# Kernel tuning notes

Hardware: AMD Instinct MI355X
Metric: run time of the kernel (lower is better)

Reference implementation:

```python
import jax, jax.numpy as jnp
import numpy as np

N_HEADS = 16
D_MODEL = 1024
D_HEAD = D_MODEL // N_HEADS


def setup_inputs() -> dict:
    key = jax.random.key(0)
    k1, k2, k3 = jax.random.split(key, 3)
    b, t, d = 2, 2048, D_MODEL
    x = jax.random.normal(k1, (b, t, d), dtype=jnp.float32)
    # Linear weights stored as [in, out] so y = x @ W (equivalent to torch's x @ W.T)
    w_qkv = jax.random.normal(k2, (d, 3 * d), dtype=jnp.float32) * (1.0 / np.sqrt(d))
    w_out = jax.random.normal(k3, (d, d), dtype=jnp.float32) * (1.0 / np.sqrt(d))
    return {"x": x, "w_qkv": w_qkv, "w_out": w_out}


def reference(x, w_qkv, w_out):
    b, t, d = x.shape
    h, dh = N_HEADS, D_HEAD
    qkv = x @ w_qkv                                   # (b, t, 3d)
    q, k, v = jnp.split(qkv, 3, axis=-1)
    # (b, h, t, dh)
    q = q.reshape(b, t, h, dh).transpose(0, 2, 1, 3)
    k = k.reshape(b, t, h, dh).transpose(0, 2, 1, 3)
    v = v.reshape(b, t, h, dh).transpose(0, 2, 1, 3)
    scale = 1.0 / np.sqrt(dh).astype(np.float32)
    att = jnp.einsum('bhqd,bhkd->bhqk', q, k) * scale  # (b, h, t, t)
    causal = jnp.tril(jnp.ones((t, t), dtype=bool))
    att = jnp.where(causal, att, -jnp.inf)
    att = jax.nn.softmax(att, axis=-1)
    y = jnp.einsum('bhqk,bhkd->bhqd', att, v)          # (b, h, t, dh)
    y = y.transpose(0, 2, 1, 3).reshape(b, t, d)
    return y @ w_out
```

## Files before the change

kernel.cpp:

```cpp
#include <hip/hip_runtime.h>
#include <hip/hip_bf16.h>
#include <stdint.h>

typedef __bf16 bf16x8 __attribute__((ext_vector_type(8)));
typedef float  f32x4  __attribute__((ext_vector_type(4)));

#define B_   2
#define T_   2048
#define H_   16
#define DH_  64
#define DM_  1024
#define BH_  (B_*H_)
#define M_   (B_*T_)

#define QSCALE 0.18033688f
#define FIXED_M 8.0f

static __device__ __forceinline__ void gload_lds16(const void* g, void* lds) {
  __builtin_amdgcn_global_load_lds(
      (const __attribute__((address_space(1))) void*)(uintptr_t)g,
      (__attribute__((address_space(3))) void*)(uint32_t)(uintptr_t)lds,
      16, 0, 0);
}

__global__ void k_cvt_bf16(const float* __restrict__ in, __hip_bfloat16* __restrict__ out, int n4) {
  int i = blockIdx.x * blockDim.x + threadIdx.x;
  if (i < n4) {
    float4 v = reinterpret_cast<const float4*>(in)[i];
    alignas(8) __hip_bfloat16 t[4] = {__float2bfloat16(v.x), __float2bfloat16(v.y),
                                      __float2bfloat16(v.z), __float2bfloat16(v.w)};
    reinterpret_cast<uint2*>(out)[i] = *reinterpret_cast<const uint2*>(t);
  }
}

__global__ void k_cvtT(const float* __restrict__ in, __hip_bfloat16* __restrict__ out, int K, int N) {
  __shared__ float tile[32][33];
  int n0 = blockIdx.x * 32, k0 = blockIdx.y * 32;
  int tid = threadIdx.x;
  int kl = tid >> 3, n4 = (tid & 7) * 4;
  float4 v = *reinterpret_cast<const float4*>(in + (size_t)(k0 + kl) * N + n0 + n4);
  tile[kl][n4 + 0] = v.x; tile[kl][n4 + 1] = v.y; tile[kl][n4 + 2] = v.z; tile[kl][n4 + 3] = v.w;
  __syncthreads();
  int nl = tid >> 3, k4 = (tid & 7) * 4;
  alignas(8) __hip_bfloat16 t[4];
  #pragma unroll
  for (int j = 0; j < 4; ++j) t[j] = __float2bfloat16(tile[k4 + j][nl]);
  *reinterpret_cast<uint2*>(out + (size_t)(n0 + nl) * K + k0 + k4) = *reinterpret_cast<const uint2*>(t);
}

template<int BM, int BN, int FM, int FN>
static __device__ __forceinline__ void gemm_core(
    const __hip_bfloat16* __restrict__ A, const __hip_bfloat16* __restrict__ BT,
    int K, int brow, int bcol, __hip_bfloat16* As, __hip_bfloat16* Bs, f32x4 acc[FM][FN]) {
  constexpr int WGN = BN / (16 * FN);
  const int tid = threadIdx.x, wave = tid >> 6, lane = tid & 63;
  const int wr = wave / WGN, wc = wave % WGN;
  const int llo = lane & 15, lhi = lane >> 4;
  for (int k0 = 0; k0 < K; k0 += 32) {
    #pragma unroll
    for (int c = wave; c < BM / 16; c += 4)
      gload_lds16(A + (size_t)(brow + c * 16 + (lane >> 2)) * K + k0 + (lane & 3) * 8,
                  As + c * 16 * 32);
    #pragma unroll
    for (int c = wave; c < BN / 16; c += 4)
      gload_lds16(BT + (size_t)(bcol + c * 16 + (lane >> 2)) * K + k0 + (lane & 3) * 8,
                  Bs + c * 16 * 32);
    __syncthreads();
    bf16x8 a[FM], b[FN];
    #pragma unroll
    for (int i = 0; i < FM; ++i)
      a[i] = *reinterpret_cast<const bf16x8*>(As + (wr * FM * 16 + i * 16 + llo) * 32 + lhi * 8);
    #pragma unroll
    for (int j = 0; j < FN; ++j)
      b[j] = *reinterpret_cast<const bf16x8*>(Bs + (wc * FN * 16 + j * 16 + llo) * 32 + lhi * 8);
    #pragma unroll
    for (int i = 0; i < FM; ++i)
      #pragma unroll
      for (int j = 0; j < FN; ++j)
        acc[i][j] = __builtin_amdgcn_mfma_f32_16x16x32_bf16(a[i], b[j], acc[i][j], 0, 0, 0);
    __syncthreads();
  }
}

__global__ __launch_bounds__(256) void k_gemm_qkv(
    const __hip_bfloat16* __restrict__ A, const __hip_bfloat16* __restrict__ BT,
    __hip_bfloat16* __restrict__ q_ws, __hip_bfloat16* __restrict__ k_ws,
    __hip_bfloat16* __restrict__ vT) {
  alignas(16) __shared__ __hip_bfloat16 As[128 * 32];
  alignas(16) __shared__ __hip_bfloat16 Bs[128 * 32];
  f32x4 acc[4][4] = {};
  const int brow = blockIdx.y * 128, bcol = blockIdx.x * 128;
  gemm_core<128, 128, 4, 4>(A, BT, DM_, brow, bcol, As, Bs, acc);
  const int tid = threadIdx.x, wave = tid >> 6, lane = tid & 63;
  const int wr = wave >> 1, wc = wave & 1;
  const int llo = lane & 15, lhi = lane >> 4;
  #pragma unroll
  for (int i = 0; i < 4; ++i) {
    const int tbase = brow + wr * 64 + i * 16 + lhi * 4;
    const int b = tbase >> 11, t = tbase & 2047;
    #pragma unroll
    for (int j = 0; j < 4; ++j) {
      int n = bcol + wc * 64 + j * 16 + llo;
      int part = n >> 10, rem = n & 1023, hh = rem >> 6, dh = rem & 63;
      if (part == 2) {
        alignas(8) __hip_bfloat16 tv[4];
        #pragma unroll
        for (int r = 0; r < 4; ++r) tv[r] = __float2bfloat16(acc[i][j][r]);
        *reinterpret_cast<uint2*>(
            vT + (((size_t)(b * H_ + hh)) * DH_ + dh) * T_ + t) =
            *reinterpret_cast<const uint2*>(tv);
      } else {
        float sc = (part == 0) ? QSCALE : 1.0f;
        __hip_bfloat16* dst = (part == 0) ? q_ws : k_ws;
        #pragma unroll
        for (int r = 0; r < 4; ++r)
          dst[(((size_t)(b * H_ + hh)) * T_ + t + r) * DH_ + dh] =
              __float2bfloat16(acc[i][j][r] * sc);
      }
    }
  }
}

__global__ __launch_bounds__(256) void k_gemm_out(
    const __hip_bfloat16* __restrict__ A, const __hip_bfloat16* __restrict__ BT,
    float* __restrict__ C) {
  alignas(16) __shared__ __hip_bfloat16 As[128 * 32];
  alignas(16) __shared__ __hip_bfloat16 Bs[64 * 32];
  f32x4 acc[4][2] = {};
  const int brow = blockIdx.y * 128, bcol = blockIdx.x * 64;
  gemm_core<128, 64, 4, 2>(A, BT, DM_, brow, bcol, As, Bs, acc);
  const int tid = threadIdx.x, wave = tid >> 6, lane = tid & 63;
  const int wr = wave >> 1, wc = wave & 1;
  const int llo = lane & 15, lhi = lane >> 4;
  #pragma unroll
  for (int i = 0; i < 4; ++i)
    #pragma unroll
    for (int j = 0; j < 2; ++j) {
      int n = bcol + wc * 32 + j * 16 + llo;
      #pragma unroll
      for (int r = 0; r < 4; ++r) {
        int m = brow + wr * 64 + i * 16 + lhi * 4 + r;
        C[(size_t)m * DM_ + n] = acc[i][j][r];
      }
    }
}

static __device__ __forceinline__ void attn_tile(
    const __hip_bfloat16* ksb, const __hip_bfloat16* vsb, __hip_bfloat16* PsW,
    const bf16x8* aq, int llo, int lhi, int qbase, int tile, bool do_mask,
    f32x4* o, float* lrow) {
  f32x4 s[4];
  __builtin_amdgcn_s_setprio(1);
  #pragma unroll
  for (int jn = 0; jn < 4; ++jn) {
    const __hip_bfloat16* krow = ksb + (jn * 16 + llo) * 64;
    bf16x8 b0 = *reinterpret_cast<const bf16x8*>(krow + ((lhi ^ (llo & 7)) << 3));
    bf16x8 b1 = *reinterpret_cast<const bf16x8*>(krow + (((4 + lhi) ^ (llo & 7)) << 3));
    f32x4 z = {};
    z = __builtin_amdgcn_mfma_f32_16x16x32_bf16(aq[0], b0, z, 0, 0, 0);
    z = __builtin_amdgcn_mfma_f32_16x16x32_bf16(aq[1], b1, z, 0, 0, 0);
    s[jn] = z;
  }
  __builtin_amdgcn_s_setprio(0);
  if (do_mask) {
    #pragma unroll
    for (int jn = 0; jn < 4; ++jn)
      #pragma unroll
      for (int r = 0; r < 4; ++r) {
        int qrow = qbase + lhi * 4 + r;
        int tcol = tile * 64 + jn * 16 + llo;
        if (tcol > qrow) s[jn][r] = -INFINITY;
      }
  }
  #pragma unroll
  for (int jn = 0; jn < 4; ++jn)
    #pragma unroll
    for (int r = 0; r < 4; ++r) {
      float pv = __builtin_amdgcn_exp2f(s[jn][r] - FIXED_M);
      lrow[r] += pv;
      int row = lhi * 4 + r, col = jn * 16 + llo;
      PsW[row * 64 + (col ^ ((row & 7) << 3))] = __float2bfloat16(pv);
    }
  bf16x8 ap0 = *reinterpret_cast<const bf16x8*>(&PsW[llo * 64 + ((lhi ^ (llo & 7)) << 3)]);
  bf16x8 ap1 = *reinterpret_cast<const bf16x8*>(&PsW[llo * 64 + (((4 + lhi) ^ (llo & 7)) << 3)]);
  __builtin_amdgcn_s_setprio(1);
  #pragma unroll
  for (int jd = 0; jd < 4; ++jd) {
    const __hip_bfloat16* vrow = vsb + (jd * 16 + llo) * 64;
    bf16x8 b0 = *reinterpret_cast<const bf16x8*>(vrow + ((lhi ^ (llo & 7)) << 3));
    bf16x8 b1 = *reinterpret_cast<const bf16x8*>(vrow + (((4 + lhi) ^ (llo & 7)) << 3));
    o[jd] = __builtin_amdgcn_mfma_f32_16x16x32_bf16(ap0, b0, o[jd], 0, 0, 0);
    o[jd] = __builtin_amdgcn_mfma_f32_16x16x32_bf16(ap1, b1, o[jd], 0, 0, 0);
  }
  __builtin_amdgcn_s_setprio(0);
}

__global__ __launch_bounds__(512, 4) void k_attn(
    const __hip_bfloat16* __restrict__ Q, const __hip_bfloat16* __restrict__ Kk,
    const __hip_bfloat16* __restrict__ VT, __hip_bfloat16* __restrict__ Y) {
  alignas(16) __shared__ __hip_bfloat16 Ks[4][64 * 64];
  alignas(16) __shared__ __hip_bfloat16 Vs[4][64 * 64];
  alignas(16) __shared__ __hip_bfloat16 Ps[8][16 * 64];
  const int bh = blockIdx.y;
  const int p  = blockIdx.x;
  const int tid = threadIdx.x, wave = tid >> 6, lane = tid & 63;
  const int llo = lane & 15, lhi = lane >> 4;
  const int group = wave >> 2, ws = wave & 3;
  const int qtA = 31 - p, qtB = p;
  const int qt_own = group ? qtB : qtA;
  const int qb_own  = qt_own * 64 + ws * 16;
  const int qb_help = qtA * 64 + ws * 16;

  const __hip_bfloat16* kb = Kk + (size_t)bh * T_ * DH_;
  const __hip_bfloat16* vb = VT + (size_t)bh * DH_ * T_;

  const int srow = lane >> 3;
  const int schunk = (lane & 7) ^ srow;
  const int rbase = ws * 16;

  auto seq = [&](int j) -> int {
    if (group == 0) return (j <= 16) ? j : -1;
    if (j <= p) return j;
    if (j <= 15) return 32 - j;
    return -1;
  };
  auto stage = [&](int tile, int slot) {
    gload_lds16(kb + (size_t)(tile * 64 + rbase + srow) * DH_ + schunk * 8,
                &Ks[slot][rbase * 64]);
    gload_lds16(kb + (size_t)(tile * 64 + rbase + 8 + srow) * DH_ + schunk * 8,
                &Ks[slot][(rbase + 8) * 64]);
    gload_lds16(vb + (size_t)(rbase + srow) * T_ + tile * 64 + schunk * 8,
                &Vs[slot][rbase * 64]);
    gload_lds16(vb + (size_t)(rbase + 8 + srow) * T_ + tile * 64 + schunk * 8,
                &Vs[slot][(rbase + 8) * 64]);
  };

  bf16x8 aq_own[2], aq_help[2];
  #pragma unroll
  for (int k0 = 0; k0 < 2; ++k0) {
    aq_own[k0] = *reinterpret_cast<const bf16x8*>(
        Q + ((size_t)bh * T_ + qb_own + llo) * DH_ + k0 * 32 + lhi * 8);
    aq_help[k0] = *reinterpret_cast<const bf16x8*>(
        Q + ((size_t)bh * T_ + qb_help + llo) * DH_ + k0 * 32 + lhi * 8);
  }

  float l_own[4] = {0.f, 0.f, 0.f, 0.f}, l_help[4] = {0.f, 0.f, 0.f, 0.f};
  f32x4 o_own[4] = {}, o_help[4] = {};

  stage(0, group * 2);
  __syncthreads();

  for (int j = 0; j <= 16; ++j) {
    const int s1 = seq(j + 1);
    if (s1 >= 0) stage(s1, group * 2 + ((j + 1) & 1));
    const int tc = seq(j);
    if (tc >= 0) {
      const __hip_bfloat16* ksb = &Ks[group * 2 + (j & 1)][0];
      const __hip_bfloat16* vsb = &Vs[group * 2 + (j & 1)][0];
      if (group == 0 || j <= p)
        attn_tile(ksb, vsb, &Ps[wave][0], aq_own, llo, lhi, qb_own, tc,
                  tc == qt_own, o_own, l_own);
      else
        attn_tile(ksb, vsb, &Ps[wave][0], aq_help, llo, lhi, qb_help, tc,
                  tc == qtA, o_help, l_help);
    }
    __syncthreads();
  }

  float* Oh = reinterpret_cast<float*>(&Ks[0][0]);
  float* Lh = reinterpret_cast<float*>(&Vs[0][0]);
  if (group == 1) {
    #pragma unroll
    for (int r = 0; r < 4; ++r) {
      float lh = l_help[r];
      #pragma unroll
      for (int d = 1; d < 16; d <<= 1) lh += __shfl_xor(lh, d);
      if (llo == 0) Lh[ws * 16 + lhi * 4 + r] = lh;
    }
    #pragma unroll
    for (int jd = 0; jd < 4; ++jd)
      #pragma unroll
      for (int r = 0; r < 4; ++r)
        Oh[ws * 1024 + (lhi * 4 + r) * 64 + jd * 16 + llo] = o_help[jd][r];
  }
  __syncthreads();

  float lr[4];
  #pragma unroll
  for (int r = 0; r < 4; ++r) {
    float ps = l_own[r];
    #pragma unroll
    for (int d = 1; d < 16; d <<= 1) ps += __shfl_xor(ps, d);
    lr[r] = ps;
  }
  if (group == 0) {
    #pragma unroll
    for (int r = 0; r < 4; ++r) lr[r] += Lh[ws * 16 + lhi * 4 + r];
    #pragma unroll
    for (int jd = 0; jd < 4; ++jd)
      #pragma unroll
      for (int r = 0; r < 4; ++r)
        o_own[jd][r] += Oh[ws * 1024 + (lhi * 4 + r) * 64 + jd * 16 + llo];
  }

  const int b = bh >> 4, h = bh & 15;
  #pragma unroll
  for (int jd = 0; jd < 4; ++jd)
    #pragma unroll
    for (int r = 0; r < 4; ++r) {
      int trow = qb_own + lhi * 4 + r;
      int col = h * 64 + jd * 16 + llo;
      Y[((size_t)(b * T_ + trow)) * DM_ + col] = __float2bfloat16(o_own[jd][r] / lr[r]);
    }
}

extern "C" void kernel_launch(void* const* d_in, const int* in_sizes, int n_in,
                              void* d_out, int out_size, void* d_ws, size_t ws_size,
                              hipStream_t stream) {
  const float* x     = (const float*)d_in[0];
  const float* w_qkv = (const float*)d_in[1];
  const float* w_out = (const float*)d_in[2];
  float* out = (float*)d_out;
  char* ws = (char*)d_ws;

  size_t off = 0;
  __hip_bfloat16* xb    = (__hip_bfloat16*)(ws + off); off += (size_t)M_ * DM_ * 2;
  __hip_bfloat16* wqkvT = (__hip_bfloat16*)(ws + off); off += (size_t)3 * DM_ * DM_ * 2;
  __hip_bfloat16* woutT = (__hip_bfloat16*)(ws + off); off += (size_t)DM_ * DM_ * 2;
  __hip_bfloat16* q_ws  = (__hip_bfloat16*)(ws + off); off += (size_t)M_ * DM_ * 2;
  __hip_bfloat16* k_ws  = (__hip_bfloat16*)(ws + off); off += (size_t)M_ * DM_ * 2;
  __hip_bfloat16* vT    = (__hip_bfloat16*)(ws + off); off += (size_t)M_ * DM_ * 2;
  __hip_bfloat16* y_ws  = (__hip_bfloat16*)(ws + off); off += (size_t)M_ * DM_ * 2;
  (void)ws_size; (void)in_sizes; (void)n_in; (void)out_size;

  k_cvt_bf16<<<(M_ * DM_ / 4 + 255) / 256, 256, 0, stream>>>(x, xb, M_ * DM_ / 4);
  k_cvtT<<<dim3(3 * DM_ / 32, DM_ / 32), 256, 0, stream>>>(w_qkv, wqkvT, DM_, 3 * DM_);
  k_cvtT<<<dim3(DM_ / 32, DM_ / 32), 256, 0, stream>>>(w_out, woutT, DM_, DM_);

  k_gemm_qkv<<<dim3(3 * DM_ / 128, M_ / 128), 256, 0, stream>>>(xb, wqkvT, q_ws, k_ws, vT);

  k_attn<<<dim3(T_ / 128, BH_), 512, 0, stream>>>(q_ws, k_ws, vT, y_ws);

  k_gemm_out<<<dim3(DM_ / 64, M_ / 128), 256, 0, stream>>>(y_ws, woutT, out);
}
```

Before: 113.7 us.

## Give each attention wave 32 query rows and remap blocks to XCDs

The attention kernel now runs with 256 threads (4 waves) per block. Each wave handles two 16-row query fragments, so every K/V fragment read from LDS is reused across 32 query rows, which halves LDS reads per unit of MFMA work. The flat grid is also remapped so that blocks sharing a given head land on the same XCD, with the aim of better L2 locality for K and V. In exchange, register pressure goes up (launch bounds change to 256,2), there are fewer waves per block, and the P tile round-trips through LDS twice per tile.

```diff
diff --git a/kernel.cpp b/kernel.cpp
--- a/kernel.cpp
+++ b/kernel.cpp
@@ -145,78 +145,29 @@
     }
 }
 
-static __device__ __forceinline__ void attn_tile(
-    const __hip_bfloat16* ksb, const __hip_bfloat16* vsb, __hip_bfloat16* PsW,
-    const bf16x8* aq, int llo, int lhi, int qbase, int tile, bool do_mask,
-    f32x4* o, float* lrow) {
-  f32x4 s[4];
-  __builtin_amdgcn_s_setprio(1);
-  #pragma unroll
-  for (int jn = 0; jn < 4; ++jn) {
-    const __hip_bfloat16* krow = ksb + (jn * 16 + llo) * 64;
-    bf16x8 b0 = *reinterpret_cast<const bf16x8*>(krow + ((lhi ^ (llo & 7)) << 3));
-    bf16x8 b1 = *reinterpret_cast<const bf16x8*>(krow + (((4 + lhi) ^ (llo & 7)) << 3));
-    f32x4 z = {};
-    z = __builtin_amdgcn_mfma_f32_16x16x32_bf16(aq[0], b0, z, 0, 0, 0);
-    z = __builtin_amdgcn_mfma_f32_16x16x32_bf16(aq[1], b1, z, 0, 0, 0);
-    s[jn] = z;
-  }
-  __builtin_amdgcn_s_setprio(0);
-  if (do_mask) {
-    #pragma unroll
-    for (int jn = 0; jn < 4; ++jn)
-      #pragma unroll
-      for (int r = 0; r < 4; ++r) {
-        int qrow = qbase + lhi * 4 + r;
-        int tcol = tile * 64 + jn * 16 + llo;
-        if (tcol > qrow) s[jn][r] = -INFINITY;
-      }
-  }
-  #pragma unroll
-  for (int jn = 0; jn < 4; ++jn)
-    #pragma unroll
-    for (int r = 0; r < 4; ++r) {
-      float pv = __builtin_amdgcn_exp2f(s[jn][r] - FIXED_M);
-      lrow[r] += pv;
-      int row = lhi * 4 + r, col = jn * 16 + llo;
-      PsW[row * 64 + (col ^ ((row & 7) << 3))] = __float2bfloat16(pv);
-    }
-  bf16x8 ap0 = *reinterpret_cast<const bf16x8*>(&PsW[llo * 64 + ((lhi ^ (llo & 7)) << 3)]);
-  bf16x8 ap1 = *reinterpret_cast<const bf16x8*>(&PsW[llo * 64 + (((4 + lhi) ^ (llo & 7)) << 3)]);
-  __builtin_amdgcn_s_setprio(1);
-  #pragma unroll
-  for (int jd = 0; jd < 4; ++jd) {
-    const __hip_bfloat16* vrow = vsb + (jd * 16 + llo) * 64;
-    bf16x8 b0 = *reinterpret_cast<const bf16x8*>(vrow + ((lhi ^ (llo & 7)) << 3));
-    bf16x8 b1 = *reinterpret_cast<const bf16x8*>(vrow + (((4 + lhi) ^ (llo & 7)) << 3));
-    o[jd] = __builtin_amdgcn_mfma_f32_16x16x32_bf16(ap0, b0, o[jd], 0, 0, 0);
-    o[jd] = __builtin_amdgcn_mfma_f32_16x16x32_bf16(ap1, b1, o[jd], 0, 0, 0);
-  }
-  __builtin_amdgcn_s_setprio(0);
-}
-
-__global__ __launch_bounds__(512, 4) void k_attn(
+__global__ __launch_bounds__(256, 2) void k_attn(
     const __hip_bfloat16* __restrict__ Q, const __hip_bfloat16* __restrict__ Kk,
     const __hip_bfloat16* __restrict__ VT, __hip_bfloat16* __restrict__ Y) {
-  alignas(16) __shared__ __hip_bfloat16 Ks[4][64 * 64];
-  alignas(16) __shared__ __hip_bfloat16 Vs[4][64 * 64];
-  alignas(16) __shared__ __hip_bfloat16 Ps[8][16 * 64];
-  const int bh = blockIdx.y;
-  const int p  = blockIdx.x;
+  alignas(16) __shared__ __hip_bfloat16 Ks[2][2][64 * 64];
+  alignas(16) __shared__ __hip_bfloat16 Vs[2][2][64 * 64];
+  alignas(16) __shared__ __hip_bfloat16 Ps[4][16 * 64];
+  const int bid = blockIdx.x;
+  const int xcd = bid & 7, idx = bid >> 3;
+  const int bh = ((idx & 3) << 3) | xcd;
+  const int p  = idx >> 2;
   const int tid = threadIdx.x, wave = tid >> 6, lane = tid & 63;
   const int llo = lane & 15, lhi = lane >> 4;
-  const int group = wave >> 2, ws = wave & 3;
+  const int group = wave >> 1, wg = wave & 1;
   const int qtA = 31 - p, qtB = p;
   const int qt_own = group ? qtB : qtA;
-  const int qb_own  = qt_own * 64 + ws * 16;
-  const int qb_help = qtA * 64 + ws * 16;
+  const int qr_own  = qt_own * 64 + wg * 32;
+  const int qr_help = qtA * 64 + wg * 32;
 
   const __hip_bfloat16* kb = Kk + (size_t)bh * T_ * DH_;
   const __hip_bfloat16* vb = VT + (size_t)bh * DH_ * T_;
 
   const int srow = lane >> 3;
   const int schunk = (lane & 7) ^ srow;
-  const int rbase = ws * 16;
 
   auto seq = [&](int j) -> int {
     if (group == 0) return (j <= 16) ? j : -1;
@@ -224,94 +175,177 @@
     if (j <= 15) return 32 - j;
     return -1;
   };
-  auto stage = [&](int tile, int slot) {
-    gload_lds16(kb + (size_t)(tile * 64 + rbase + srow) * DH_ + schunk * 8,
-                &Ks[slot][rbase * 64]);
-    gload_lds16(kb + (size_t)(tile * 64 + rbase + 8 + srow) * DH_ + schunk * 8,
-                &Ks[slot][(rbase + 8) * 64]);
-    gload_lds16(vb + (size_t)(rbase + srow) * T_ + tile * 64 + schunk * 8,
-                &Vs[slot][rbase * 64]);
-    gload_lds16(vb + (size_t)(rbase + 8 + srow) * T_ + tile * 64 + schunk * 8,
-                &Vs[slot][(rbase + 8) * 64]);
+  auto stage = [&](int tile, int slt) {
+    #pragma unroll
+    for (int g = 0; g < 4; ++g) {
+      const int rb = wg * 32 + g * 8;
+      gload_lds16(kb + (size_t)(tile * 64 + rb + srow) * DH_ + schunk * 8,
+                  &Ks[group][slt][rb * 64]);
+      gload_lds16(vb + (size_t)(rb + srow) * T_ + tile * 64 + schunk * 8,
+                  &Vs[group][slt][rb * 64]);
+    }
   };
 
-  bf16x8 aq_own[2], aq_help[2];
-  #pragma unroll
-  for (int k0 = 0; k0 < 2; ++k0) {
-    aq_own[k0] = *reinterpret_cast<const bf16x8*>(
-        Q + ((size_t)bh * T_ + qb_own + llo) * DH_ + k0 * 32 + lhi * 8);
-    aq_help[k0] = *reinterpret_cast<const bf16x8*>(
-        Q + ((size_t)bh * T_ + qb_help + llo) * DH_ + k0 * 32 + lhi * 8);
-  }
-
-  float l_own[4] = {0.f, 0.f, 0.f, 0.f}, l_help[4] = {0.f, 0.f, 0.f, 0.f};
-  f32x4 o_own[4] = {}, o_help[4] = {};
-
-  stage(0, group * 2);
+  bf16x8 aq_own[2][2], aq_help[2][2];
+  #pragma unroll
+  for (int f = 0; f < 2; ++f)
+    #pragma unroll
+    for (int k0 = 0; k0 < 2; ++k0) {
+      aq_own[f][k0] = *reinterpret_cast<const bf16x8*>(
+          Q + ((size_t)bh * T_ + qr_own + f * 16 + llo) * DH_ + k0 * 32 + lhi * 8);
+      aq_help[f][k0] = *reinterpret_cast<const bf16x8*>(
+          Q + ((size_t)bh * T_ + qr_help + f * 16 + llo) * DH_ + k0 * 32 + lhi * 8);
+    }
+
+  float l_own[2][4] = {}, l_help[2][4] = {};
+  f32x4 o_own[2][4] = {}, o_help[2][4] = {};
+
+  stage(0, 0);
   __syncthreads();
 
   for (int j = 0; j <= 16; ++j) {
     const int s1 = seq(j + 1);
-    if (s1 >= 0) stage(s1, group * 2 + ((j + 1) & 1));
+    if (s1 >= 0) stage(s1, (j + 1) & 1);
     const int tc = seq(j);
     if (tc >= 0) {
-      const __hip_bfloat16* ksb = &Ks[group * 2 + (j & 1)][0];
-      const __hip_bfloat16* vsb = &Vs[group * 2 + (j & 1)][0];
-      if (group == 0 || j <= p)
-        attn_tile(ksb, vsb, &Ps[wave][0], aq_own, llo, lhi, qb_own, tc,
-                  tc == qt_own, o_own, l_own);
-      else
-        attn_tile(ksb, vsb, &Ps[wave][0], aq_help, llo, lhi, qb_help, tc,
-                  tc == qtA, o_help, l_help);
+      const __hip_bfloat16* ksb = &Ks[group][j & 1][0];
+      const __hip_bfloat16* vsb = &Vs[group][j & 1][0];
+      const bool own = (group == 0) || (j <= p);
+      const bf16x8 (*aq)[2] = own ? aq_own : aq_help;
+      f32x4 (*o)[4]  = own ? o_own : o_help;
+      float (*lr)[4] = own ? l_own : l_help;
+      const int qb = own ? qr_own : qr_help;
+      const int qt = own ? qt_own : qtA;
+
+      f32x4 s[2][4];
+      __builtin_amdgcn_s_setprio(1);
+      #pragma unroll
+      for (int jn = 0; jn < 4; ++jn) {
+        const __hip_bfloat16* krow = ksb + (jn * 16 + llo) * 64;
+        bf16x8 b0 = *reinterpret_cast<const bf16x8*>(krow + ((lhi ^ (llo & 7)) << 3));
+        bf16x8 b1 = *reinterpret_cast<const bf16x8*>(krow + (((4 + lhi) ^ (llo & 7)) << 3));
+        #pragma unroll
+        for (int f = 0; f < 2; ++f) {
+          f32x4 z = {};
+          z = __builtin_amdgcn_mfma_f32_16x16x32_bf16(aq[f][0], b0, z, 0, 0, 0);
+          z = __builtin_amdgcn_mfma_f32_16x16x32_bf16(aq[f][1], b1, z, 0, 0, 0);
+          s[f][jn] = z;
+        }
+      }
+      __builtin_amdgcn_s_setprio(0);
+      if (tc == qt) {
+        #pragma unroll
+        for (int f = 0; f < 2; ++f)
+          #pragma unroll
+          for (int jn = 0; jn < 4; ++jn)
+            #pragma unroll
+            for (int r = 0; r < 4; ++r) {
+              int qrow = qb + f * 16 + lhi * 4 + r;
+              int tcol = tc * 64 + jn * 16 + llo;
+              if (tcol > qrow) s[f][jn][r] = -INFINITY;
+            }
+      }
+      #pragma unroll
+      for (int f = 0; f < 2; ++f)
+        #pragma unroll
+        for (int jn = 0; jn < 4; ++jn)
+          #pragma unroll
+          for (int r = 0; r < 4; ++r) {
+            float pv = __builtin_amdgcn_exp2f(s[f][jn][r] - FIXED_M);
+            s[f][jn][r] = pv;
+            lr[f][r] += pv;
+          }
+      bf16x8 vb0[4], vb1[4];
+      #pragma unroll
+      for (int jd = 0; jd < 4; ++jd) {
+        const __hip_bfloat16* vrow = vsb + (jd * 16 + llo) * 64;
+        vb0[jd] = *reinterpret_cast<const bf16x8*>(vrow + ((lhi ^ (llo & 7)) << 3));
+        vb1[jd] = *reinterpret_cast<const bf16x8*>(vrow + (((4 + lhi) ^ (llo & 7)) << 3));
+      }
+      #pragma unroll
+      for (int f = 0; f < 2; ++f) {
+        #pragma unroll
+        for (int jn = 0; jn < 4; ++jn)
+          #pragma unroll
+          for (int r = 0; r < 4; ++r) {
+            int row = lhi * 4 + r, col = jn * 16 + llo;
+            Ps[wave][row * 64 + (col ^ ((row & 7) << 3))] = __float2bfloat16(s[f][jn][r]);
+          }
+        bf16x8 ap0 = *reinterpret_cast<const bf16x8*>(
+            &Ps[wave][llo * 64 + ((lhi ^ (llo & 7)) << 3)]);
+        bf16x8 ap1 = *reinterpret_cast<const bf16x8*>(
+            &Ps[wave][llo * 64 + (((4 + lhi) ^ (llo & 7)) << 3)]);
+        __builtin_amdgcn_s_setprio(1);
+        #pragma unroll
+        for (int jd = 0; jd < 4; ++jd) {
+          o[f][jd] = __builtin_amdgcn_mfma_f32_16x16x32_bf16(ap0, vb0[jd], o[f][jd], 0, 0, 0);
+          o[f][jd] = __builtin_amdgcn_mfma_f32_16x16x32_bf16(ap1, vb1[jd], o[f][jd], 0, 0, 0);
+        }
+        __builtin_amdgcn_s_setprio(0);
+      }
     }
     __syncthreads();
   }
 
-  float* Oh = reinterpret_cast<float*>(&Ks[0][0]);
-  float* Lh = reinterpret_cast<float*>(&Vs[0][0]);
+  float* Oh = reinterpret_cast<float*>(&Ks[0][0][0]);
+  float* Lh = reinterpret_cast<float*>(&Vs[0][0][0]);
   if (group == 1) {
     #pragma unroll
+    for (int f = 0; f < 2; ++f)
+      #pragma unroll
+      for (int r = 0; r < 4; ++r) {
+        float lh = l_help[f][r];
+        #pragma unroll
+        for (int d = 1; d < 16; d <<= 1) lh += __shfl_xor(lh, d);
+        if (llo == 0) Lh[wg * 32 + f * 16 + lhi * 4 + r] = lh;
+      }
+    #pragma unroll
+    for (int f = 0; f < 2; ++f)
+      #pragma unroll
+      for (int jd = 0; jd < 4; ++jd)
+        #pragma unroll
+        for (int r = 0; r < 4; ++r)
+          Oh[(wg * 32 + f * 16 + lhi * 4 + r) * 64 + jd * 16 + llo] = o_help[f][jd][r];
+  }
+  __syncthreads();
+
+  float lfin[2][4];
+  #pragma unroll
+  for (int f = 0; f < 2; ++f)
+    #pragma unroll
     for (int r = 0; r < 4; ++r) {
-      float lh = l_help[r];
-      #pragma unroll
-      for (int d = 1; d < 16; d <<= 1) lh += __shfl_xor(lh, d);
-      if (llo == 0) Lh[ws * 16 + lhi * 4 + r] = lh;
-    }
+      float ps = l_own[f][r];
+      #pragma unroll
+      for (int d = 1; d < 16; d <<= 1) ps += __shfl_xor(ps, d);
+      lfin[f][r] = ps;
+    }
+  if (group == 0) {
+    #pragma unroll
+    for (int f = 0; f < 2; ++f)
+      #pragma unroll
+      for (int r = 0; r < 4; ++r)
+        lfin[f][r] += Lh[wg * 32 + f * 16 + lhi * 4 + r];
+    #pragma unroll
+    for (int f = 0; f < 2; ++f)
+      #pragma unroll
+      for (int jd = 0; jd < 4; ++jd)
+        #pragma unroll
+        for (int r = 0; r < 4; ++r)
+          o_own[f][jd][r] += Oh[(wg * 32 + f * 16 + lhi * 4 + r) * 64 + jd * 16 + llo];
+  }
+
+  const int b = bh >> 4, h = bh & 15;
+  #pragma unroll
+  for (int f = 0; f < 2; ++f)
     #pragma unroll
     for (int jd = 0; jd < 4; ++jd)
       #pragma unroll
-      for (int r = 0; r < 4; ++r)
-        Oh[ws * 1024 + (lhi * 4 + r) * 64 + jd * 16 + llo] = o_help[jd][r];
-  }
-  __syncthreads();
-
-  float lr[4];
-  #pragma unroll
-  for (int r = 0; r < 4; ++r) {
-    float ps = l_own[r];
-    #pragma unroll
-    for (int d = 1; d < 16; d <<= 1) ps += __shfl_xor(ps, d);
-    lr[r] = ps;
-  }
-  if (group == 0) {
-    #pragma unroll
-    for (int r = 0; r < 4; ++r) lr[r] += Lh[ws * 16 + lhi * 4 + r];
-    #pragma unroll
-    for (int jd = 0; jd < 4; ++jd)
-      #pragma unroll
-      for (int r = 0; r < 4; ++r)
-        o_own[jd][r] += Oh[ws * 1024 + (lhi * 4 + r) * 64 + jd * 16 + llo];
-  }
-
-  const int b = bh >> 4, h = bh & 15;
-  #pragma unroll
-  for (int jd = 0; jd < 4; ++jd)
-    #pragma unroll
-    for (int r = 0; r < 4; ++r) {
-      int trow = qb_own + lhi * 4 + r;
-      int col = h * 64 + jd * 16 + llo;
-      Y[((size_t)(b * T_ + trow)) * DM_ + col] = __float2bfloat16(o_own[jd][r] / lr[r]);
-    }
+      for (int r = 0; r < 4; ++r) {
+        int trow = qr_own + f * 16 + lhi * 4 + r;
+        int col = h * 64 + jd * 16 + llo;
+        Y[((size_t)(b * T_ + trow)) * DM_ + col] =
+            __float2bfloat16(o_own[f][jd][r] / lfin[f][r]);
+      }
 }
 
 extern "C" void kernel_launch(void* const* d_in, const int* in_sizes, int n_in,
@@ -339,7 +373,7 @@
 
   k_gemm_qkv<<<dim3(3 * DM_ / 128, M_ / 128), 256, 0, stream>>>(xb, wqkvT, q_ws, k_ws, vT);
 
-  k_attn<<<dim3(T_ / 128, BH_), 512, 0, stream>>>(q_ws, k_ws, vT, y_ws);
+  k_attn<<<dim3(512), 256, 0, stream>>>(q_ws, k_ws, vT, y_ws);
 
   k_gemm_out<<<dim3(DM_ / 64, M_ / 128), 256, 0, stream>>>(y_ws, woutT, out);
 }
```

After: 119.6 us. +5.2%, slower.
